# Kernel optimization log

Measured on AMD Instinct MI355X. Metric: run time of the kernel, lower is better.

Reference implementation:

```python
import jax, jax.numpy as jnp
import numpy as np

B, S, H = 1, 2048, 4096
NH, NKV, HD = 32, 8, 128
GROUP = NH // NKV  # 4
SCALE = 0.08838834764831845  # 1/sqrt(head_dim)
ROPE_BASE = 10000.0


def setup_inputs() -> dict:
    key = jax.random.key(0)
    k1, k2, k3 = jax.random.split(key, 3)
    hidden_states = jax.random.normal(k1, (B, S, H), jnp.float32)
    # c_attn: [H + 2*NKV*HD, H] = [6144, 4096]; c_proj: [H, H]
    w_attn = jax.random.normal(k2, (H + 2 * NKV * HD, H), jnp.float32) * 0.02
    w_proj = jax.random.normal(k3, (H, H), jnp.float32) * (0.02 / np.sqrt(2 * 32))
    # standard rotate-half RoPE tables, shape [S, HD]
    inv_freq = 1.0 / (ROPE_BASE ** (jnp.arange(0, HD, 2, dtype=jnp.float32) / HD))
    freqs = jnp.outer(jnp.arange(S, dtype=jnp.float32), inv_freq)
    emb = jnp.concatenate([freqs, freqs], axis=-1)
    return {
        "hidden_states": hidden_states,
        "w_attn": w_attn,
        "w_proj": w_proj,
        "rope_cos": jnp.cos(emb),
        "rope_sin": jnp.sin(emb),
    }


def _apply_rope(x, cos, sin):
    # x: [B, heads, S, HD]; cos/sin: [S, HD] broadcast over batch/heads
    x1, x2 = jnp.split(x, 2, axis=-1)
    rot = jnp.concatenate([-x2, x1], axis=-1)
    return x * cos + rot * sin


def reference(hidden_states, w_attn, w_proj, rope_cos, rope_sin):
    b, s, _ = hidden_states.shape
    # fused QKV projection (no bias)
    qkv = hidden_states @ w_attn.T  # [B, S, H + 2*NKV*HD]
    qkv = qkv.reshape(b, s, NKV, (GROUP + 2) * HD)
    q = qkv[..., : GROUP * HD].reshape(b, s, NH, HD)
    k = qkv[..., GROUP * HD : (GROUP + 1) * HD]  # [B, S, NKV, HD]
    v = qkv[..., (GROUP + 1) * HD :]
    q = q.transpose(0, 2, 1, 3)  # [B, NH, S, HD]
    k = k.transpose(0, 2, 1, 3)  # [B, NKV, S, HD]
    v = v.transpose(0, 2, 1, 3)
    q = _apply_rope(q, rope_cos, rope_sin)
    k = _apply_rope(k, rope_cos, rope_sin)
    # GQA: group query heads per kv head instead of repeating K/V
    qg = q.reshape(b, NKV, GROUP, s, HD)
    scores = jnp.einsum("bkgqd,bksd->bkgqs", qg, k) * SCALE
    causal = jnp.tril(jnp.ones((s, s), dtype=bool))
    scores = jnp.where(causal, scores, jnp.finfo(scores.dtype).min)
    probs = jax.nn.softmax(scores, axis=-1)
    out = jnp.einsum("bkgqs,bksd->bkgqd", probs, v)
    out = out.reshape(b, NH, s, HD).transpose(0, 2, 1, 3).reshape(b, s, NH * HD)
    return out @ w_proj.T
```

## Files before the change

### kernel.cpp

```cpp
#include <hip/hip_runtime.h>
#include <cstdint>
#include <cstddef>

typedef __attribute__((ext_vector_type(4))) float f32x4;
typedef __attribute__((ext_vector_type(8))) short bf16x8;

#define S_LEN 2048
#define HDIM 4096
#define QKVD 6144
#define NHEAD 32
#define NKVH 8
#define HD 128
#define QPRE 0.12751744631123533f

__device__ __forceinline__ short f2bf(float f) {
  unsigned int u = __float_as_uint(f);
  u += 0x7FFFu + ((u >> 16) & 1u);
  return (short)(u >> 16);
}
__device__ __forceinline__ float bf2f(short s) {
  return __uint_as_float((unsigned int)(unsigned short)s << 16);
}

__device__ __forceinline__ void gl_lds16(const short* g, short* l) {
  __builtin_amdgcn_global_load_lds((const __attribute__((address_space(1))) void*)g,
                                   (__attribute__((address_space(3))) void*)l,
                                   16, 0, 0);
}

template<int N> __device__ __forceinline__ void vmw() {
  if constexpr (N == 0) asm volatile("s_waitcnt vmcnt(0)" ::: "memory");
  else if constexpr (N == 1) asm volatile("s_waitcnt vmcnt(1)" ::: "memory");
  else if constexpr (N == 2) asm volatile("s_waitcnt vmcnt(2)" ::: "memory");
  else if constexpr (N == 3) asm volatile("s_waitcnt vmcnt(3)" ::: "memory");
  else if constexpr (N == 4) asm volatile("s_waitcnt vmcnt(4)" ::: "memory");
}

__global__ void cvt3_kernel(const float* __restrict__ a, short* __restrict__ oa, int na,
                            const float* __restrict__ b, short* __restrict__ ob, int nb,
                            const float* __restrict__ c, short* __restrict__ oc, int nc) {
  int i = (blockIdx.x * blockDim.x + threadIdx.x) * 4;
  const float* src; short* dst;
  if (i < na) { src = a + i; dst = oa + i; }
  else if (i < na + nb) { src = b + (i - na); dst = ob + (i - na); }
  else if (i < na + nb + nc) { src = c + (i - na - nb); dst = oc + (i - na - nb); }
  else return;
  const float4 v = *reinterpret_cast<const float4*>(src);
  short4 o;
  o.x = f2bf(v.x); o.y = f2bf(v.y); o.z = f2bf(v.z); o.w = f2bf(v.w);
  *reinterpret_cast<short4*>(dst) = o;
}

#define PHASE(MH, NH, LOADA, LOADB, VM, STAGE) { \
    if (LOADA) { const short* bA = lA + buf * ATILE; \
      _Pragma("unroll") for (int m = 0; m < 2; ++m) { \
        int row = wm * 64 + (MH) * 32 + m * 16 + l15; \
        _Pragma("unroll") for (int kk = 0; kk < 2; ++kk) { \
          int slot = ((kk << 2) + l4) ^ (row & 7); \
          afH[m][kk] = *reinterpret_cast<const bf16x8*>(bA + row * 64 + slot * 8); } } } \
    if (LOADB) { const short* bB = lB + buf * BTILE; \
      _Pragma("unroll") for (int n = 0; n < NQ; ++n) { \
        int row = wn * (BN >> 2) + n * 32 + (NH) * 16 + l15; \
        _Pragma("unroll") for (int kk = 0; kk < 2; ++kk) { \
          int slot = ((kk << 2) + l4) ^ (row & 7); \
          bfH[n][kk] = *reinterpret_cast<const bf16x8*>(bB + row * 64 + slot * 8); } } } \
    STAGE; \
    vmw<(VM)>(); \
    __builtin_amdgcn_s_barrier(); \
    __builtin_amdgcn_sched_barrier(0); \
    __builtin_amdgcn_s_setprio(1); \
    _Pragma("unroll") for (int m = 0; m < 2; ++m) \
      _Pragma("unroll") for (int n = 0; n < NQ; ++n) \
        _Pragma("unroll") for (int kk = 0; kk < 2; ++kk) \
          acc[(MH) * 2 + m][(NH) * NQ + n] = __builtin_amdgcn_mfma_f32_16x16x32_bf16( \
              afH[m][kk], bfH[n][kk], acc[(MH) * 2 + m][(NH) * NQ + n], 0, 0, 0); \
    __builtin_amdgcn_s_setprio(0); }

template<int BN>
__global__ __launch_bounds__(512, 2) void gemm8p(const short* __restrict__ A,
                                                 const short* __restrict__ B,
                                                 float* __restrict__ C,
                                                 int M, int N, int K) {
  extern __shared__ short sm[];
  constexpr int NQ = BN / 128;
  constexpr int ATILE = 128 * 64;
  constexpr int BTILE = BN * 64;
  const int tid = threadIdx.x;
  const int wv = tid >> 6, lane = tid & 63;
  const int wm = wv >> 2, wn = wv & 3;
  const int l15 = lane & 15, l4 = lane >> 4;
  const int nbn = N / BN;
  const int nwg = gridDim.x;
  const int bid = blockIdx.x;
  const int sbid = (bid & 7) * (nwg >> 3) + (bid >> 3);
  const int tm = (sbid / nbn) * 128, tn = (sbid % nbn) * BN;
  short* lA = sm;
  short* lB = sm + 2 * ATILE;
  (void)M;

  f32x4 acc[4][2 * NQ] = {};
  bf16x8 afH[2][2], bfH[NQ][2];

  auto stageA = [&](int k0, int bufi, int sel) {
    short* dst = lA + bufi * ATILE;
    int rowIdx = tid >> 3;
    int row = (rowIdx >> 5) * 64 + sel * 32 + (rowIdx & 31);
    int slot = tid & 7;
    gl_lds16(A + (size_t)(tm + row) * K + k0 + ((slot ^ (row & 7)) << 3),
             dst + row * 64 + slot * 8);
  };
  auto stageB = [&](int k0, int bufi, int par) {
    short* dst = lB + bufi * BTILE;
#pragma unroll
    for (int j = 0; j < NQ; ++j) {
      int rowIdx = (tid >> 3) + j * 64;
      int row = (rowIdx >> 4) * 32 + par * 16 + (rowIdx & 15);
      int slot = tid & 7;
      gl_lds16(B + (size_t)(tn + row) * K + k0 + ((slot ^ (row & 7)) << 3),
               dst + row * 64 + slot * 8);
    }
  };

  stageA(0, 0, 0);
  stageB(0, 0, 0);
  stageB(0, 0, 1);
  stageA(0, 0, 1);
  vmw<NQ + 1>();
  __builtin_amdgcn_s_barrier();
  __builtin_amdgcn_sched_barrier(0);

  const int KT = K >> 6;
  for (int t = 0; t < KT - 1; ++t) {
    const int buf = t & 1, nbuf = buf ^ 1, nk0 = (t + 1) << 6;
    PHASE(0, 0, 1, 1, 2,      stageA(nk0, nbuf, 0))
    PHASE(0, 1, 0, 1, NQ + 1, stageB(nk0, nbuf, 0))
    PHASE(1, 1, 1, 0, 99,     stageB(nk0, nbuf, 1))
    PHASE(1, 0, 0, 1, NQ + 1, stageA(nk0, nbuf, 1))
  }
  {
    const int buf = (KT - 1) & 1;
    PHASE(0, 0, 1, 1, 1,  (void)0)
    PHASE(0, 1, 0, 1, 0,  (void)0)
    PHASE(1, 1, 1, 0, 99, (void)0)
    PHASE(1, 0, 0, 1, 99, (void)0)
  }
#pragma unroll
  for (int mg = 0; mg < 4; ++mg)
#pragma unroll
    for (int NH = 0; NH < 2; ++NH)
#pragma unroll
      for (int n = 0; n < NQ; ++n)
#pragma unroll
        for (int r = 0; r < 4; ++r) {
          int row = tm + wm * 64 + mg * 16 + l4 * 4 + r;
          int col = tn + wn * (BN >> 2) + n * 32 + NH * 16 + l15;
          C[(size_t)row * N + col] = acc[mg][NH * NQ + n][r];
        }
}

__global__ void rope2_kernel(const float* __restrict__ qkv,
                             const float* __restrict__ cb,
                             const float* __restrict__ sb,
                             short* __restrict__ Q,
                             short* __restrict__ Kx) {
  int tid = blockIdx.x * blockDim.x + threadIdx.x;
  int dh = tid & 63;
  int t2 = tid >> 6;
  int part = t2 % 5;
  int t3 = t2 / 5;
  int g = t3 & 7;
  int s = t3 >> 3;
  const float* base = qkv + (size_t)s * QKVD + g * 768 + part * 128;
  float v1 = base[dh], v2 = base[dh + 64];
  float c = cb[s * HD + dh], sn = sb[s * HD + dh];
  float o1 = v1 * c - v2 * sn;
  float o2 = v2 * c + v1 * sn;
  if (part < 4) {
    o1 *= QPRE; o2 *= QPRE;
    short* dst = Q + ((size_t)(g * 4 + part) * S_LEN + s) * HD;
    dst[dh] = f2bf(o1);
    dst[dh + 64] = f2bf(o2);
  } else {
    short* dst = Kx + ((size_t)g * S_LEN + s) * HD;
    dst[dh] = f2bf(o1);
    dst[dh + 64] = f2bf(o2);
  }
}

__global__ __launch_bounds__(256) void vtrans2_kernel(const float* __restrict__ qkv,
                                                      short* __restrict__ Vt) {
  __shared__ short tile[64][72];
  const int kvh = blockIdx.z;
  const int s0 = blockIdx.x * 64, d0 = blockIdx.y * 64;
  const int t = threadIdx.x;
#pragma unroll
  for (int i = 0; i < 4; ++i) {
    int c = t + i * 256;
    int sl = c >> 4, dl = (c & 15) * 4;
    const float4 v = *reinterpret_cast<const float4*>(
        qkv + (size_t)(s0 + sl) * QKVD + kvh * 768 + 640 + d0 + dl);
    tile[sl][dl] = f2bf(v.x); tile[sl][dl + 1] = f2bf(v.y);
    tile[sl][dl + 2] = f2bf(v.z); tile[sl][dl + 3] = f2bf(v.w);
  }
  __syncthreads();
  short* Vtb = Vt + (size_t)kvh * HD * S_LEN;
#pragma unroll
  for (int i = 0; i < 2; ++i) {
    int dl = i * 32 + (t >> 3), sl = (t & 7) * 8;
    bf16x8 o;
#pragma unroll
    for (int j = 0; j < 8; ++j) o[j] = tile[sl + j][dl];
    *reinterpret_cast<bf16x8*>(Vtb + (size_t)(d0 + dl) * S_LEN + s0 + sl) = o;
  }
}

__global__ __launch_bounds__(256, 2) void attn_kernel(const short* __restrict__ Q,
                                                      const short* __restrict__ Kx,
                                                      const short* __restrict__ Vt,
                                                      short* __restrict__ part0,
                                                      short* __restrict__ part1,
                                                      float2* __restrict__ stat0,
                                                      float2* __restrict__ stat1) {
  __shared__ short lK[2 * 64 * 128];
  __shared__ unsigned int lPu[4 * 2 * 512];
  const int tt = threadIdx.x;
  const int w = tt >> 6, lane = tt & 63;
  const int l15 = lane & 15, l4 = lane >> 4;
  const int kvh = blockIdx.x;
  const int qt = 63 - blockIdx.y;
  const int z = blockIdx.z;
  const int h = kvh * 4 + w;
  short* pout = z ? part1 : part0;
  float2* sout = z ? stat1 : stat0;

  const int nkt = (qt >> 1) + 1;
  const int ts = (nkt + 1) >> 1;
  const int t0 = z ? ts : 0;
  const int t1 = z ? nkt : ts;

  f32x4 o[2][8] = {};
  float m_run[2] = {-1e30f, -1e30f};
  float lsum[2] = {0.f, 0.f};

  if (t0 < t1) {
    bf16x8 qf[2][4];
#pragma unroll
    for (int qa = 0; qa < 2; ++qa) {
      const short* qrow = Q + ((size_t)h * S_LEN + qt * 32 + qa * 16 + l15) * HD + l4 * 8;
#pragma unroll
      for (int fd = 0; fd < 4; ++fd)
        qf[qa][fd] = *reinterpret_cast<const bf16x8*>(qrow + fd * 32);
    }
    const short* Kb = Kx + (size_t)kvh * S_LEN * HD;
    const short* Vb = Vt + (size_t)kvh * HD * S_LEN;

    {
      const short* Kg = Kb + (size_t)(t0 * 64) * HD;
#pragma unroll
      for (int i = 0; i < 4; ++i) {
        int c = tt + i * 256, row = c >> 4, jj = (c & 15) ^ (row & 7);
        gl_lds16(Kg + (size_t)row * HD + jj * 8, lK + c * 8);
      }
    }
    __syncthreads();

    int cur = 0;
    for (int kt = t0; kt < t1; ++kt) {
      const int c0 = kt * 64;
      if (kt + 1 < t1) {
        const short* Kg = Kb + (size_t)(c0 + 64) * HD;
        short* dst = lK + (cur ^ 1) * (64 * 128);
#pragma unroll
        for (int i = 0; i < 4; ++i) {
          int c = tt + i * 256, row = c >> 4, jj = (c & 15) ^ (row & 7);
          gl_lds16(Kg + (size_t)row * HD + jj * 8, dst + c * 8);
        }
      }
      const short* src = lK + cur * (64 * 128);
      f32x4 sf[2][4] = {};
      __builtin_amdgcn_s_setprio(1);
#pragma unroll
      for (int n = 0; n < 4; ++n) {
        bf16x8 kf[4];
#pragma unroll
        for (int fd = 0; fd < 4; ++fd) {
          int row = n * 16 + l15, jp = (l4 + fd * 4) ^ (l15 & 7);
          kf[fd] = *reinterpret_cast<const bf16x8*>(src + row * 128 + jp * 8);
        }
#pragma unroll
        for (int fd = 0; fd < 4; ++fd) {
          sf[0][n] = __builtin_amdgcn_mfma_f32_16x16x32_bf16(kf[fd], qf[0][fd], sf[0][n], 0, 0, 0);
          sf[1][n] = __builtin_amdgcn_mfma_f32_16x16x32_bf16(kf[fd], qf[1][fd], sf[1][n], 0, 0, 0);
        }
      }
      __builtin_amdgcn_s_setprio(0);
      bf16x8 vreg[8][2];
#pragma unroll
      for (int fd = 0; fd < 8; ++fd) {
        const short* vrow = Vb + (size_t)(fd * 16 + l15) * S_LEN + c0 + l4 * 8;
        vreg[fd][0] = *reinterpret_cast<const bf16x8*>(vrow);
        vreg[fd][1] = *reinterpret_cast<const bf16x8*>(vrow + 32);
      }
      const bool lastt = (kt == nkt - 1);
#pragma unroll
      for (int qa = 0; qa < 2; ++qa) {
        if (lastt) {
          const int qrow_g = qt * 32 + qa * 16 + l15;
#pragma unroll
          for (int n = 0; n < 4; ++n)
#pragma unroll
            for (int r = 0; r < 4; ++r)
              if ((c0 + n * 16 + l4 * 4 + r) > qrow_g) sf[qa][n][r] = -1e30f;
        }
        float mx = sf[qa][0][0];
#pragma unroll
        for (int n = 0; n < 4; ++n)
#pragma unroll
          for (int r = 0; r < 4; ++r) mx = fmaxf(mx, sf[qa][n][r]);
        mx = fmaxf(mx, __shfl_xor(mx, 16, 64));
        mx = fmaxf(mx, __shfl_xor(mx, 32, 64));
        float mnew = fmaxf(m_run[qa], mx);
        float alpha = exp2f(m_run[qa] - mnew);
        m_run[qa] = mnew;
        float ps = 0.f;
#pragma unroll
        for (int n = 0; n < 4; ++n)
#pragma unroll
          for (int r = 0; r < 4; ++r) {
            float e = exp2f(sf[qa][n][r] - mnew);
            sf[qa][n][r] = e;
            ps += e;
          }
        lsum[qa] = lsum[qa] * alpha + ps;
#pragma unroll
        for (int n = 0; n < 4; ++n)
#pragma unroll
          for (int rp = 0; rp < 2; ++rp) {
            unsigned int pkv =
                ((unsigned int)(unsigned short)f2bf(sf[qa][n][rp * 2 + 1]) << 16) |
                (unsigned short)f2bf(sf[qa][n][rp * 2]);
            int kv5 = ((n & 1) << 4) + l4 * 4 + rp * 2;
            lPu[w * 1024 + qa * 512 + ((n >> 1) << 8) +
                (l15 + ((kv5 >> 3) << 4)) * 4 + ((kv5 & 7) >> 1)] = pkv;
          }
        float aO[4];
#pragma unroll
        for (int r = 0; r < 4; ++r) aO[r] = __shfl(alpha, l4 * 4 + r, 64);
#pragma unroll
        for (int fd = 0; fd < 8; ++fd) {
          o[qa][fd][0] *= aO[0]; o[qa][fd][1] *= aO[1];
          o[qa][fd][2] *= aO[2]; o[qa][fd][3] *= aO[3];
        }
      }
      asm volatile("s_waitcnt lgkmcnt(0)" ::: "memory");
      bf16x8 pf[2][2];
#pragma unroll
      for (int qa = 0; qa < 2; ++qa)
#pragma unroll
        for (int p = 0; p < 2; ++p)
          pf[qa][p] = *reinterpret_cast<const bf16x8*>(
              (const short*)lPu + (w * 1024 + qa * 512 + p * 256 + lane * 4) * 2);
      __builtin_amdgcn_s_setprio(1);
#pragma unroll
      for (int fd = 0; fd < 8; ++fd) {
        o[0][fd] = __builtin_amdgcn_mfma_f32_16x16x32_bf16(pf[0][0], vreg[fd][0], o[0][fd], 0, 0, 0);
        o[0][fd] = __builtin_amdgcn_mfma_f32_16x16x32_bf16(pf[0][1], vreg[fd][1], o[0][fd], 0, 0, 0);
        o[1][fd] = __builtin_amdgcn_mfma_f32_16x16x32_bf16(pf[1][0], vreg[fd][0], o[1][fd], 0, 0, 0);
        o[1][fd] = __builtin_amdgcn_mfma_f32_16x16x32_bf16(pf[1][1], vreg[fd][1], o[1][fd], 0, 0, 0);
      }
      __builtin_amdgcn_s_setprio(0);
      __syncthreads();
      cur ^= 1;
    }
  }
#pragma unroll
  for (int qa = 0; qa < 2; ++qa) {
    float s = lsum[qa];
    s += __shfl_xor(s, 16, 64);
    s += __shfl_xor(s, 32, 64);
    if (l4 == 0)
      sout[(size_t)h * S_LEN + qt * 32 + qa * 16 + l15] = make_float2(m_run[qa], s);
#pragma unroll
    for (int fd = 0; fd < 8; ++fd)
#pragma unroll
      for (int r = 0; r < 4; ++r)
        pout[((size_t)h * S_LEN + qt * 32 + qa * 16 + l4 * 4 + r) * HD + fd * 16 + l15] =
            f2bf(o[qa][fd][r]);
  }
}

__global__ __launch_bounds__(256) void combine_kernel(const short* __restrict__ p0,
                                                      const short* __restrict__ p1,
                                                      const float2* __restrict__ st0,
                                                      const float2* __restrict__ st1,
                                                      short* __restrict__ AO) {
  int idx = (blockIdx.x * 256 + threadIdx.x) * 8;
  int h = idx >> 18;
  int rem = idx & ((1 << 18) - 1);
  int s = rem >> 7, d = rem & 127;
  float2 a = st0[(size_t)h * S_LEN + s];
  float2 b = st1[(size_t)h * S_LEN + s];
  float M = fmaxf(a.x, b.x);
  float w0 = exp2f(a.x - M), w1 = exp2f(b.x - M);
  float inv = 1.f / (a.y * w0 + b.y * w1);
  w0 *= inv; w1 *= inv;
  bf16x8 v0 = *reinterpret_cast<const bf16x8*>(p0 + idx);
  bf16x8 v1 = *reinterpret_cast<const bf16x8*>(p1 + idx);
  bf16x8 ov;
#pragma unroll
  for (int j = 0; j < 8; ++j)
    ov[j] = f2bf(bf2f(v0[j]) * w0 + bf2f(v1[j]) * w1);
  *reinterpret_cast<bf16x8*>(AO + (size_t)s * HDIM + h * HD + d) = ov;
}

extern "C" void kernel_launch(void* const* d_in, const int* in_sizes, int n_in,
                              void* d_out, int out_size, void* d_ws, size_t ws_size,
                              hipStream_t stream) {
  const float* hidden = (const float*)d_in[0];
  const float* w_attn = (const float*)d_in[1];
  const float* w_proj = (const float*)d_in[2];
  const float* rcos = (const float*)d_in[3];
  const float* rsin = (const float*)d_in[4];
  float* out = (float*)d_out;
  char* ws = (char*)d_ws;

  short* Xb  = (short*)(ws);
  short* Wab = (short*)(ws + (16u << 20));
  short* Qb  = (short*)(ws + (16u << 20));
  short* Kb  = (short*)(ws + (32u << 20));
  short* Vtb = (short*)(ws + (36u << 20));
  float2* St0 = (float2*)(ws + (40u << 20));
  float2* St1 = (float2*)(ws + (41u << 20));
  short* Pt0 = (short*)(ws + (44u << 20));
  float* QKVf = (float*)(ws + (64u << 20));
  short* Pt1 = (short*)(ws + (64u << 20));
  short* Wpb = (short*)(ws + (80u << 20));
  short* AO  = Xb;

  const int nX = S_LEN * HDIM;
  const int nWa = QKVD * HDIM;
  const int nWp = HDIM * HDIM;

  hipFuncSetAttribute(reinterpret_cast<const void*>(gemm8p<384>),
                      hipFuncAttributeMaxDynamicSharedMemorySize, 131072);
  hipFuncSetAttribute(reinterpret_cast<const void*>(gemm8p<256>),
                      hipFuncAttributeMaxDynamicSharedMemorySize, 98304);

  cvt3_kernel<<<(nX + nWa) / 1024, 256, 0, stream>>>(
      hidden, Xb, nX, w_attn, Wab, nWa, (const float*)nullptr, (short*)nullptr, 0);
  gemm8p<384><<<256, 512, 131072, stream>>>(Xb, Wab, QKVf, S_LEN, QKVD, HDIM);
  rope2_kernel<<<(S_LEN * NKVH * 5 * 64) / 256, 256, 0, stream>>>(QKVf, rcos, rsin, Qb, Kb);
  vtrans2_kernel<<<dim3(S_LEN / 64, HD / 64, NKVH), 256, 0, stream>>>(QKVf, Vtb);
  cvt3_kernel<<<nWp / 1024, 256, 0, stream>>>(
      w_proj, Wpb, nWp, (const float*)nullptr, (short*)nullptr, 0,
      (const float*)nullptr, (short*)nullptr, 0);
  attn_kernel<<<dim3(NKVH, 64, 2), 256, 0, stream>>>(Qb, Kb, Vtb, Pt0, Pt1, St0, St1);
  combine_kernel<<<(NHEAD * S_LEN * HD / 8) / 256, 256, 0, stream>>>(Pt0, Pt1, St0, St1, AO);
  gemm8p<256><<<256, 512, 98304, stream>>>(AO, Wpb, out, S_LEN, HDIM, HDIM);
}
```

Measured before the change: 332.0 us.

## Restructure GEMM K-loop from four phases to two per tile

Collapses the four-phase per-K-tile schedule (each loading a quarter of A/B fragments and issuing one barrier) into two phases. Each phase loads all B fragments and half of A, issues two global-to-LDS stage ops, and runs twice as many MFMAs between barriers. The aim is to halve barrier and wait overhead and lengthen MFMA runs. In exchange it holds more B fragment registers (bfH doubled), which may pressure occupancy at 2 blocks/CU, and it overlaps global loads with compute more coarsely.

```diff
diff --git a/kernel.cpp b/kernel.cpp
--- a/kernel.cpp
+++ b/kernel.cpp
@@ -51,29 +51,51 @@
   *reinterpret_cast<short4*>(dst) = o;
 }
 
-#define PHASE(MH, NH, LOADA, LOADB, VM, STAGE) { \
-    if (LOADA) { const short* bA = lA + buf * ATILE; \
+#define PHASE2A(VM, STAGE1, STAGE2) { \
+    { const short* bA = lA + buf * ATILE; \
       _Pragma("unroll") for (int m = 0; m < 2; ++m) { \
-        int row = wm * 64 + (MH) * 32 + m * 16 + l15; \
+        int row = wm * 64 + m * 16 + l15; \
         _Pragma("unroll") for (int kk = 0; kk < 2; ++kk) { \
           int slot = ((kk << 2) + l4) ^ (row & 7); \
           afH[m][kk] = *reinterpret_cast<const bf16x8*>(bA + row * 64 + slot * 8); } } } \
-    if (LOADB) { const short* bB = lB + buf * BTILE; \
-      _Pragma("unroll") for (int n = 0; n < NQ; ++n) { \
-        int row = wn * (BN >> 2) + n * 32 + (NH) * 16 + l15; \
-        _Pragma("unroll") for (int kk = 0; kk < 2; ++kk) { \
-          int slot = ((kk << 2) + l4) ^ (row & 7); \
-          bfH[n][kk] = *reinterpret_cast<const bf16x8*>(bB + row * 64 + slot * 8); } } } \
-    STAGE; \
+    { const short* bB = lB + buf * BTILE; \
+      _Pragma("unroll") for (int nh = 0; nh < 2; ++nh) \
+        _Pragma("unroll") for (int n = 0; n < NQ; ++n) { \
+          int row = wn * (BN >> 2) + n * 32 + nh * 16 + l15; \
+          _Pragma("unroll") for (int kk = 0; kk < 2; ++kk) { \
+            int slot = ((kk << 2) + l4) ^ (row & 7); \
+            bfH[nh][n][kk] = *reinterpret_cast<const bf16x8*>(bB + row * 64 + slot * 8); } } } \
+    STAGE1; STAGE2; \
     vmw<(VM)>(); \
     __builtin_amdgcn_s_barrier(); \
     __builtin_amdgcn_sched_barrier(0); \
     __builtin_amdgcn_s_setprio(1); \
     _Pragma("unroll") for (int m = 0; m < 2; ++m) \
-      _Pragma("unroll") for (int n = 0; n < NQ; ++n) \
-        _Pragma("unroll") for (int kk = 0; kk < 2; ++kk) \
-          acc[(MH) * 2 + m][(NH) * NQ + n] = __builtin_amdgcn_mfma_f32_16x16x32_bf16( \
-              afH[m][kk], bfH[n][kk], acc[(MH) * 2 + m][(NH) * NQ + n], 0, 0, 0); \
+      _Pragma("unroll") for (int nh = 0; nh < 2; ++nh) \
+        _Pragma("unroll") for (int n = 0; n < NQ; ++n) \
+          _Pragma("unroll") for (int kk = 0; kk < 2; ++kk) \
+            acc[m][nh * NQ + n] = __builtin_amdgcn_mfma_f32_16x16x32_bf16( \
+                afH[m][kk], bfH[nh][n][kk], acc[m][nh * NQ + n], 0, 0, 0); \
+    __builtin_amdgcn_s_setprio(0); }
+
+#define PHASE2B(VM, STAGE1, STAGE2) { \
+    { const short* bA = lA + buf * ATILE; \
+      _Pragma("unroll") for (int m = 0; m < 2; ++m) { \
+        int row = wm * 64 + 32 + m * 16 + l15; \
+        _Pragma("unroll") for (int kk = 0; kk < 2; ++kk) { \
+          int slot = ((kk << 2) + l4) ^ (row & 7); \
+          afH[m][kk] = *reinterpret_cast<const bf16x8*>(bA + row * 64 + slot * 8); } } } \
+    STAGE1; STAGE2; \
+    vmw<(VM)>(); \
+    __builtin_amdgcn_s_barrier(); \
+    __builtin_amdgcn_sched_barrier(0); \
+    __builtin_amdgcn_s_setprio(1); \
+    _Pragma("unroll") for (int m = 0; m < 2; ++m) \
+      _Pragma("unroll") for (int nh = 0; nh < 2; ++nh) \
+        _Pragma("unroll") for (int n = 0; n < NQ; ++n) \
+          _Pragma("unroll") for (int kk = 0; kk < 2; ++kk) \
+            acc[2 + m][nh * NQ + n] = __builtin_amdgcn_mfma_f32_16x16x32_bf16( \
+                afH[m][kk], bfH[nh][n][kk], acc[2 + m][nh * NQ + n], 0, 0, 0); \
     __builtin_amdgcn_s_setprio(0); }
 
 template<int BN>
@@ -99,7 +121,7 @@
   (void)M;
 
   f32x4 acc[4][2 * NQ] = {};
-  bf16x8 afH[2][2], bfH[NQ][2];
+  bf16x8 afH[2][2], bfH[2][NQ][2];
 
   auto stageA = [&](int k0, int bufi, int sel) {
     short* dst = lA + bufi * ATILE;
@@ -125,24 +147,20 @@
   stageB(0, 0, 0);
   stageB(0, 0, 1);
   stageA(0, 0, 1);
-  vmw<NQ + 1>();
+  vmw<1>();
   __builtin_amdgcn_s_barrier();
   __builtin_amdgcn_sched_barrier(0);
 
   const int KT = K >> 6;
   for (int t = 0; t < KT - 1; ++t) {
     const int buf = t & 1, nbuf = buf ^ 1, nk0 = (t + 1) << 6;
-    PHASE(0, 0, 1, 1, 2,      stageA(nk0, nbuf, 0))
-    PHASE(0, 1, 0, 1, NQ + 1, stageB(nk0, nbuf, 0))
-    PHASE(1, 1, 1, 0, 99,     stageB(nk0, nbuf, 1))
-    PHASE(1, 0, 0, 1, NQ + 1, stageA(nk0, nbuf, 1))
+    PHASE2A(NQ + 1, stageA(nk0, nbuf, 0), stageB(nk0, nbuf, 0))
+    PHASE2B(1,      stageB(nk0, nbuf, 1), stageA(nk0, nbuf, 1))
   }
   {
     const int buf = (KT - 1) & 1;
-    PHASE(0, 0, 1, 1, 1,  (void)0)
-    PHASE(0, 1, 0, 1, 0,  (void)0)
-    PHASE(1, 1, 1, 0, 99, (void)0)
-    PHASE(1, 0, 0, 1, 99, (void)0)
+    PHASE2A(0,  (void)0, (void)0)
+    PHASE2B(99, (void)0, (void)0)
   }
 #pragma unroll
   for (int mg = 0; mg < 4; ++mg)
```

After: 354.6 us. +6.8%, slower.
